# Optimization experiments

Measured on AMD Instinct MI355X. Metric: run time of the kernel, lower is better.

The kernel has to match this reference:

```python
import jax, jax.numpy as jnp
import numpy as np

N_NODES = 50000


def gcn_conv(x, W, b, edge_index, n):
    # PyG GCNConv(add_self_loops=False): h = x @ W; out[c] = sum_e norm_e * h[row_e]
    # with norm_e = deg(row)^-1/2 * deg(col)^-1/2, deg = in-degree on col.
    h = x @ W  # [N, out]
    row, col = edge_index[0], edge_index[1]
    deg = jax.ops.segment_sum(jnp.ones(row.shape, h.dtype), col, num_segments=n)
    dis = jnp.where(deg > 0, jax.lax.rsqrt(jnp.where(deg > 0, deg, 1.0)), 0.0)
    norm = dis[row] * dis[col]  # [E]
    msg = h[row] * norm[:, None]  # [E, out]
    out = jax.ops.segment_sum(msg, col, num_segments=n)
    return out + b


def setup_inputs() -> dict:
    key = jax.random.key(0)
    ks = jax.random.split(key, 12)
    N, F, H0, H1, H2, C = N_NODES, 512, 256, 128, 128, 40
    E1, E2 = 800000, 1600000
    s = 0.05
    return {
        "x": jax.random.normal(ks[0], (N, F), jnp.float32),
        "edge_index": jax.random.randint(ks[1], (2, E1), 0, N, jnp.int32),
        "edge_index2": jax.random.randint(ks[2], (2, E2), 0, N, jnp.int32),
        "W_lin1": jax.random.normal(ks[3], (F, H0), jnp.float32) * s,
        "b_lin1": jnp.zeros((H0,), jnp.float32),
        "W_c1": jax.random.normal(ks[4], (H0, H1), jnp.float32) * s,
        "b_c1": jnp.zeros((H1,), jnp.float32),
        "W_c2": jax.random.normal(ks[5], (2 * H1, H2), jnp.float32) * s,
        "b_c2": jnp.zeros((H2,), jnp.float32),
        "W_lin2": jax.random.normal(ks[6], (H0 + 2 * H1 + 2 * H2, C), jnp.float32) * s,
        "b_lin2": jnp.zeros((C,), jnp.float32),
    }


def reference(x, edge_index, edge_index2, W_lin1, b_lin1, W_c1, b_c1, W_c2, b_c2, W_lin2, b_lin2):
    n = x.shape[0]
    h = jax.nn.relu(x @ W_lin1 + b_lin1)  # [N, H0]
    first_hop_h = gcn_conv(h, W_c1, b_c1, edge_index, n)
    second_hop_h = gcn_conv(h, W_c1, b_c1, edge_index2, n)
    R1 = jnp.concatenate([first_hop_h, second_hop_h], axis=1)  # [N, 2*H1]
    first_hop_h2 = gcn_conv(R1, W_c2, b_c2, edge_index, n)
    second_hop_h2 = gcn_conv(R1, W_c2, b_c2, edge_index2, n)
    R2 = jnp.concatenate([first_hop_h2, second_hop_h2], axis=1)  # [N, 2*H2]
    final_h = jnp.concatenate([h, R1, R2], axis=1)  # [N, H0+2H1+2H2]
    # dropout treated as identity (eval / deterministic reference)
    logits = final_h @ W_lin2 + b_lin2
    return jax.nn.log_softmax(logits, axis=1)
```

## Files before the change

kernel.cpp:

```cpp
#include <hip/hip_runtime.h>
#include <hip/hip_bf16.h>
#include <stdint.h>

typedef __attribute__((ext_vector_type(8))) short bf16x8;
typedef __attribute__((ext_vector_type(8))) unsigned short ushort8v;
typedef __attribute__((ext_vector_type(4))) float f32x4;
typedef __attribute__((ext_vector_type(2))) float f32x2;
typedef __attribute__((ext_vector_type(4))) unsigned int u32x4;
typedef unsigned long long ull;

__device__ __forceinline__ void load_lds16(const void* g, void* l){
  __builtin_amdgcn_global_load_lds((const __attribute__((address_space(1))) void*)g,
                                   (__attribute__((address_space(3))) void*)l, 16, 0, 0);
}

__device__ __forceinline__ float bf2f(unsigned int u){
  union { unsigned int i; float f; } x; x.i = u << 16; return x.f;
}
__device__ __forceinline__ unsigned short f2bf(float f){
  __hip_bfloat16 h = __float2bfloat16(f);
  unsigned short u;
  __builtin_memcpy(&u, &h, 2);
  return u;
}

__global__ void wtrans4_kernel(const float* __restrict__ W1, unsigned short* __restrict__ Wt1,
                               const float* __restrict__ Wc1, unsigned short* __restrict__ Wtc1,
                               const float* __restrict__ Wc2, unsigned short* __restrict__ Wtc2,
                               const float* __restrict__ Wf, unsigned short* __restrict__ Wtf,
                               int NB, int cap1r, int cap2r, int* __restrict__ bcur,
                               unsigned* __restrict__ Tz0, unsigned* __restrict__ Tz1){
  int idx = blockIdx.x*256 + threadIdx.x;
  if (idx >= 245760){
    int i = idx - 245760;
    if (i < NB) bcur[i] = i*cap1r;
    else if (i < 2*NB) bcur[i] = NB*cap1r + (i - NB)*cap2r;
    else if (i < 2*NB + 32) Tz0[i - 2*NB] = 0u;
    else if (i < 2*NB + 64) Tz1[i - 2*NB - 32] = 0u;
    return;
  }
  const float* W; unsigned short* Wt; int K, N;
  if (idx < 131072){ W = W1; Wt = Wt1; K = 512; N = 256; }
  else if (idx < 163840){ idx -= 131072; W = Wc1; Wt = Wtc1; K = 256; N = 128; }
  else if (idx < 196608){ idx -= 163840; W = Wc2; Wt = Wtc2; K = 256; N = 128; }
  else { idx -= 196608; W = Wf; Wt = Wtf; K = 768; N = 40; }
  int nn = idx / K, kk = idx - nn*K;
  float v = (nn < N) ? W[(size_t)kk*N + nn] : 0.f;
  Wt[idx] = f2bf(v);
}

#define PCH 4096

__global__ __launch_bounds__(256) void partA_kernel(
    const int* __restrict__ ei1, int E1, const int* __restrict__ ei2, int E2,
    int* __restrict__ bcur, unsigned* __restrict__ staging, int NB)
{
  const int set = blockIdx.y;
  const int* __restrict__ ei = set ? ei2 : ei1;
  const int E = set ? E2 : E1;
  int* __restrict__ cur = bcur + set*NB;
  __shared__ int hist[400];
  __shared__ int resv[400];
  const int tid = threadIdx.x;
  const int base = blockIdx.x * PCH;
  if (base >= E) return;
  for (int b = tid; b < NB; b += 256) hist[b] = 0;
  __syncthreads();

  if (base + PCH <= E){
    const int t0 = base + tid*16;
    int4 c[4], r[4];
    #pragma unroll
    for (int j = 0; j < 4; ++j) c[j] = *(const int4*)(ei + E + t0 + j*4);
    #pragma unroll
    for (int j = 0; j < 4; ++j) r[j] = *(const int4*)(ei + t0 + j*4);
    #pragma unroll
    for (int j = 0; j < 4; ++j){
      atomicAdd(&hist[c[j].x >> 7], 1); atomicAdd(&hist[c[j].y >> 7], 1);
      atomicAdd(&hist[c[j].z >> 7], 1); atomicAdd(&hist[c[j].w >> 7], 1);
    }
    __syncthreads();
    for (int b = tid; b < NB; b += 256){
      int hc = hist[b];
      resv[b] = hc ? atomicAdd(&cur[b], hc) : 0;
      hist[b] = 0;
    }
    __syncthreads();
    #pragma unroll
    for (int j = 0; j < 4; ++j){
      int cc, rr, b, s;
      cc = c[j].x; rr = r[j].x; b = cc >> 7;
      s = resv[b] + atomicAdd(&hist[b], 1);
      staging[s] = ((unsigned)rr << 7) | (unsigned)(cc & 127);
      cc = c[j].y; rr = r[j].y; b = cc >> 7;
      s = resv[b] + atomicAdd(&hist[b], 1);
      staging[s] = ((unsigned)rr << 7) | (unsigned)(cc & 127);
      cc = c[j].z; rr = r[j].z; b = cc >> 7;
      s = resv[b] + atomicAdd(&hist[b], 1);
      staging[s] = ((unsigned)rr << 7) | (unsigned)(cc & 127);
      cc = c[j].w; rr = r[j].w; b = cc >> 7;
      s = resv[b] + atomicAdd(&hist[b], 1);
      staging[s] = ((unsigned)rr << 7) | (unsigned)(cc & 127);
    }
  } else {
    for (int i = 0; i < PCH/256; ++i){
      int e = base + i*256 + tid;
      if (e < E) atomicAdd(&hist[ei[E + e] >> 7], 1);
    }
    __syncthreads();
    for (int b = tid; b < NB; b += 256){
      int hc = hist[b];
      resv[b] = hc ? atomicAdd(&cur[b], hc) : 0;
      hist[b] = 0;
    }
    __syncthreads();
    for (int i = 0; i < PCH/256; ++i){
      int e = base + i*256 + tid;
      if (e < E){
        int c = ei[E + e], r = ei[e];
        int b = c >> 7;
        int s = resv[b] + atomicAdd(&hist[b], 1);
        staging[s] = ((unsigned)r << 7) | (unsigned)(c & 127);
      }
    }
  }
}

__global__ __launch_bounds__(256) void degB_kernel(
    const unsigned* __restrict__ staging, const int* __restrict__ bcur,
    int* __restrict__ deg1, int* __restrict__ deg2,
    float* __restrict__ dis1, float* __restrict__ dis2,
    int NB, int n, int cap1r, int cap2r)
{
  const int set = blockIdx.y;
  int* __restrict__ deg = set ? deg2 : deg1;
  float* __restrict__ dis = set ? dis2 : dis1;
  const int b = blockIdx.x;
  const int nodebase = b << 7;
  const int nn = min(128, n - nodebase);
  if (nn <= 0) return;
  __shared__ int cnt[128];
  const int tid = threadIdx.x;
  if (tid < 128) cnt[tid] = 0;
  __syncthreads();
  const int s0 = set ? (NB*cap1r + b*cap2r) : (b*cap1r);
  const int s1 = bcur[set*NB + b];
  for (int i = s0 + tid; i < s1; i += 256)
    atomicAdd(&cnt[staging[i] & 127], 1);
  __syncthreads();
  if (tid < nn){
    int c = cnt[tid];
    deg[nodebase + tid] = c;
    dis[nodebase + tid] = (c > 0) ? (1.0f/sqrtf((float)c)) : 0.f;
  }
}

__global__ void scan1_kernel(const int* __restrict__ deg1, const int* __restrict__ deg2,
                             int* __restrict__ off1, int* __restrict__ off2,
                             int* __restrict__ bsum, int n){
  __shared__ int s[1024];
  int set = blockIdx.y;
  const int* deg = set ? deg2 : deg1;
  int* off = set ? off2 : off1;
  int tid = threadIdx.x;
  int i = blockIdx.x*1024 + tid;
  int v = (i < n) ? ((deg[i] + 7) & ~7) : 0;
  s[tid] = v;
  __syncthreads();
  for (int o = 1; o < 1024; o <<= 1){
    int t = (tid >= o) ? s[tid - o] : 0;
    __syncthreads();
    s[tid] += t;
    __syncthreads();
  }
  if (i < n) off[i] = s[tid];
  if (tid == 1023) bsum[set*64 + blockIdx.x] = s[1023];
}

__global__ void scan2_kernel(const int* __restrict__ bsum, int* __restrict__ bbase,
                             int nch, int* __restrict__ off1, int* __restrict__ off2, int n){
  int set = threadIdx.x;
  if (set < 2){
    int run = 0;
    for (int j = 0; j < nch; ++j){ bbase[set*64 + j] = run; run += bsum[set*64 + j]; }
    (set ? off2 : off1)[n] = run;
  }
}

__global__ void scan3_kernel(const int* __restrict__ deg1, const int* __restrict__ deg2,
                             int* __restrict__ off1, int* __restrict__ off2,
                             const int* __restrict__ bbase, int n){
  int set = blockIdx.y;
  const int* deg = set ? deg2 : deg1;
  int* off = set ? off2 : off1;
  int i = blockIdx.x*1024 + threadIdx.x;
  if (i < n){
    int e = off[i] + bbase[set*64 + blockIdx.x];
    off[i] = e - ((deg[i] + 7) & ~7);
  }
}

__global__ __launch_bounds__(256) void partB_kernel(
    const unsigned* __restrict__ staging, const int* __restrict__ bcur,
    const int* __restrict__ off1, const int* __restrict__ off2,
    unsigned* __restrict__ csr1, unsigned* __restrict__ csr2,
    int NB, int n, unsigned padrow, int cap1r, int cap2r)
{
  const int set = blockIdx.y;
  const int* __restrict__ off = set ? off2 : off1;
  unsigned* __restrict__ csr = set ? csr2 : csr1;
  const int b = blockIdx.x;
  const int nodebase = b << 7;
  const int nn = min(128, n - nodebase);
  if (nn <= 0) return;
  __shared__ int offv[129];
  __shared__ int curl[128];
  const int tid = threadIdx.x;
  if (tid <= nn) offv[tid] = off[nodebase + tid];
  if (tid < 128) curl[tid] = 0;
  __syncthreads();
  const int s0 = set ? (NB*cap1r + b*cap2r) : (b*cap1r);
  const int s1 = bcur[set*NB + b];
  for (int i = s0 + tid; i < s1; i += 256){
    unsigned v = staging[i];
    int cl = v & 127;
    int p = offv[cl] + atomicAdd(&curl[cl], 1);
    csr[p] = v >> 7;
  }
  __syncthreads();
  for (int c = tid; c < nn; c += 256){
    int p1 = offv[c+1];
    for (int p = offv[c] + curl[c]; p < p1; ++p) csr[p] = padrow;
  }
  if (b == 0 && tid < 64) csr[off[n] + tid] = padrow;
}

#define KN 8
__global__ __launch_bounds__(256) void conv_kernel(
    const int* __restrict__ off1, const unsigned* __restrict__ csr1, const float* __restrict__ dis1,
    const int* __restrict__ off2, const unsigned* __restrict__ csr2, const float* __restrict__ dis2,
    const unsigned char* __restrict__ Tbase,
    const float* __restrict__ bias, unsigned short* __restrict__ outR,
    int n, int ntab)
{
  const int set = blockIdx.y;
  const int* __restrict__ off = set ? off2 : off1;
  const float* __restrict__ dis = set ? dis2 : dis1;
  const unsigned* __restrict__ csrq = set ? csr2 : csr1;
  const int col_ofs = set ? 128 : 0;
  const unsigned* __restrict__ tab =
      (const unsigned*)(Tbase + (size_t)set * ntab * 128);

  const int wv0 = (blockIdx.x*4 + (threadIdx.x >> 6)) * KN;
  if (wv0 >= n) return;
  const int wend = min(n, wv0 + KN);
  const int l = threadIdx.x & 63;
  const int half = l >> 5, lf = l & 31;
  const float b0 = bias[lf*4 + 0], b1 = bias[lf*4 + 1];
  const float b2 = bias[lf*4 + 2], b3 = bias[lf*4 + 3];

  const int offs = off[wv0 + min(l, wend - wv0)];
  const int cstart = __shfl(offs, 0, 64);
  const int pend   = __shfl(offs, wend - wv0, 64);
  int node = wv0;
  int nxt  = __shfl(offs, min(1, wend - wv0), 64);

  float ax = 0.f, ay = 0.f, az = 0.f, aw = 0.f;

#define EMIT_NODE { \
    float rx = ax + __shfl_xor(ax, 32, 64); \
    float ry = ay + __shfl_xor(ay, 32, 64); \
    float rz = az + __shfl_xor(az, 32, 64); \
    float rw = aw + __shfl_xor(aw, 32, 64); \
    if (half == 0){ \
      const float dc = dis[node]; \
      ull ov = (ull)((unsigned)f2bf(fmaf(dc, rx, b0)) | ((unsigned)f2bf(fmaf(dc, ry, b1)) << 16)) \
             | ((ull)((unsigned)f2bf(fmaf(dc, rz, b2)) | ((unsigned)f2bf(fmaf(dc, rw, b3)) << 16)) << 32); \
      __builtin_nontemporal_store(ov, (ull*)&outR[(size_t)node*256 + col_ofs + lf*4]); \
    } \
    ax = ay = az = aw = 0.f; }
#define DRAIN(CUR) \
    while (node < wend && (CUR) == nxt){ \
      EMIT_NODE \
      ++node; \
      nxt = __shfl(offs, min(node + 1 - wv0, KN), 64); \
    }

  DRAIN(cstart)

  const int nbat = (pend - cstart) >> 3;
  if (nbat > 0){
    const unsigned* cp = csrq + cstart + half*4;
    u32x4 qa, qb;
    unsigned va0, va1, va2, va3, vb0, vb1, vb2, vb3;

#define LQ(q, B) q = __builtin_nontemporal_load((const u32x4*)(cp + (B)*8));
#define GATH(v, q) \
    v##0 = tab[(size_t)q.x * 32 + lf]; \
    v##1 = tab[(size_t)q.y * 32 + lf]; \
    v##2 = tab[(size_t)q.z * 32 + lf]; \
    v##3 = tab[(size_t)q.w * 32 + lf];
#define FMA1(v) { \
    f32x2 lo = __builtin_amdgcn_cvt_pk_f32_fp8((int)v, false); \
    f32x2 hi = __builtin_amdgcn_cvt_pk_f32_fp8((int)v, true);  \
    ax += lo.x; ay += lo.y; az += hi.x; aw += hi.y; }
#define FMAB(v) { FMA1(v##0) FMA1(v##1) FMA1(v##2) FMA1(v##3) }

    LQ(qa, 0)
    GATH(va, qa)
    LQ(qb, 1)
    int b = 0;
    while (b + 2 <= nbat){
      LQ(qa, b + 2)
      GATH(vb, qb)
      FMAB(va)
      DRAIN(cstart + (b + 1)*8)
      LQ(qb, b + 3)
      GATH(va, qa)
      FMAB(vb)
      DRAIN(cstart + (b + 2)*8)
      b += 2;
    }
    if (b < nbat){
      FMAB(va)
      DRAIN(cstart + nbat*8)
    }
#undef LQ
#undef GATH
#undef FMA1
#undef FMAB
  }
  while (node < wend){ EMIT_NODE ++node; }
#undef EMIT_NODE
#undef DRAIN
}

template<int FM, int FN, int WGM, int WGN, int EPI, bool AF32>
__global__ __launch_bounds__(WGM*WGN*64, (WGM*WGN*64) == 512 ? 4 : 2) void gemm_kernel(
    const unsigned short* __restrict__ A0, const float* __restrict__ Af,
    const unsigned short* __restrict__ A1, const unsigned short* __restrict__ A2,
    const unsigned short* __restrict__ Bt, const float* __restrict__ bias,
    void* __restrict__ Cout, int M, int K, int lda, int ldc,
    const float* __restrict__ d1, const float* __restrict__ d2, int ntab)
{
  constexpr int THREADS = WGM*WGN*64;
  constexpr int BM = WGM*FM*16;
  constexpr int BN = WGN*FN*16;
  constexpr int BK = 32;
  constexpr int AJ = (BM*BK/8)/THREADS;
  constexpr int BJ = (BN*BK/8)/THREADS;
  static_assert(BM == 128, "staging assumes BM==128");
  __shared__ unsigned short As[BM][BK];
  __shared__ unsigned short Bs[BN][BK];
  const int tid = threadIdx.x;
  const int w = tid >> 6, l = tid & 63;
  const int wr = w / WGN, wc = w % WGN;
  const int m0 = blockIdx.x*BM, n0 = blockIdx.y*BN;
  f32x4 acc[FM][FN] = {};
  const int nsteps = K / BK;
  for (int s = 0; s < nsteps; ++s){
    const int k0 = s*BK;
    const unsigned short* Asrc = A0;
    int kin = k0;
    if constexpr (EPI == 2){
      int slab = k0 >> 8;
      Asrc = (slab == 0) ? A0 : ((slab == 1) ? A1 : A2);
      kin = k0 & 255;
    }
    __syncthreads();
    if constexpr (AF32){
      #pragma unroll
      for (int j = 0; j < AJ; ++j){
        int idx = j*THREADS + tid;
        int row = idx >> 2, kq = idx & 3;
        int rg = m0 + row; rg = (rg < M) ? rg : (M - 1);
        const float* src = Af + (size_t)rg*lda + kin + kq*8;
        float4 a = *(const float4*)src;
        float4 b2 = *(const float4*)(src + 4);
        ushort8v u;
        u[0] = f2bf(a.x);  u[1] = f2bf(a.y);  u[2] = f2bf(a.z);  u[3] = f2bf(a.w);
        u[4] = f2bf(b2.x); u[5] = f2bf(b2.y); u[6] = f2bf(b2.z); u[7] = f2bf(b2.w);
        *(ushort8v*)((char*)&As[0][0] + (size_t)idx*16) = u;
      }
    } else {
      #pragma unroll
      for (int j = 0; j < AJ; ++j){
        int idx = j*THREADS + tid;
        int row = idx >> 2, kq = idx & 3;
        int rg = m0 + row; rg = (rg < M) ? rg : (M - 1);
        load_lds16(Asrc + (size_t)rg*lda + kin + kq*8,
                   ((char*)&As[0][0]) + (size_t)(j*THREADS + w*64)*16);
      }
    }
    #pragma unroll
    for (int j = 0; j < BJ; ++j){
      int idx = j*THREADS + tid;
      int row = idx >> 2, kq = idx & 3;
      load_lds16(Bt + (size_t)(n0 + row)*K + k0 + kq*8,
                 ((char*)&Bs[0][0]) + (size_t)(j*THREADS + w*64)*16);
    }
    __syncthreads();
    bf16x8 af[FM], bfr[FN];
    const int kofs = (l >> 4)*8, l16 = l & 15;
    #pragma unroll
    for (int mi = 0; mi < FM; ++mi)
      af[mi] = *(const bf16x8*)&As[wr*FM*16 + mi*16 + l16][kofs];
    #pragma unroll
    for (int ni = 0; ni < FN; ++ni)
      bfr[ni] = *(const bf16x8*)&Bs[wc*FN*16 + ni*16 + l16][kofs];
    #pragma unroll
    for (int mi = 0; mi < FM; ++mi)
      #pragma unroll
      for (int ni = 0; ni < FN; ++ni)
        acc[mi][ni] = __builtin_amdgcn_mfma_f32_16x16x32_bf16(af[mi], bfr[ni], acc[mi][ni], 0, 0, 0);
  }
  const int lg = l >> 4, lc = l & 15;
  if constexpr (EPI == 2){
    float* O = (float*)Cout;
    #pragma unroll
    for (int mi = 0; mi < FM; ++mi){
      #pragma unroll
      for (int i = 0; i < 4; ++i){
        int row = m0 + wr*FM*16 + mi*16 + lg*4 + i;
        float v[FN];
        float mx = -1e30f;
        #pragma unroll
        for (int ni = 0; ni < FN; ++ni){
          int col = ni*16 + lc;
          v[ni] = acc[mi][ni][i] + ((col < 40) ? bias[col] : 0.f);
          if (col < 40) mx = fmaxf(mx, v[ni]);
        }
        #pragma unroll
        for (int d = 1; d < 16; d <<= 1) mx = fmaxf(mx, __shfl_xor(mx, d, 64));
        float se = 0.f;
        #pragma unroll
        for (int ni = 0; ni < FN; ++ni){
          int col = ni*16 + lc;
          if (col < 40) se += expf(v[ni] - mx);
        }
        #pragma unroll
        for (int d = 1; d < 16; d <<= 1) se += __shfl_xor(se, d, 64);
        float lse = logf(se);
        if (row < M){
          #pragma unroll
          for (int ni = 0; ni < FN; ++ni){
            int col = ni*16 + lc;
            if (col < 40) O[(size_t)row*40 + col] = v[ni] - mx - lse;
          }
        }
      }
    }
  } else if constexpr (EPI == 4){
    unsigned char* T = (unsigned char*)Cout;
    #pragma unroll
    for (int mi = 0; mi < FM; ++mi){
      #pragma unroll
      for (int i = 0; i < 4; ++i){
        int row = m0 + wr*FM*16 + mi*16 + lg*4 + i;
        if (row >= M) continue;
        float s1 = d1[row], s2 = d2[row];
        #pragma unroll
        for (int ni = 0; ni < FN; ++ni){
          int col = n0 + wc*FN*16 + ni*16 + lc;
          float vv = acc[mi][ni][i];
          unsigned p1 = (unsigned)__builtin_amdgcn_cvt_pk_fp8_f32(vv*s1, vv*s1, 0, false);
          unsigned p2 = (unsigned)__builtin_amdgcn_cvt_pk_fp8_f32(vv*s2, vv*s2, 0, false);
          T[(size_t)row*128 + col] = (unsigned char)(p1 & 0xff);
          T[((size_t)ntab + row)*128 + col] = (unsigned char)(p2 & 0xff);
        }
      }
    }
  } else {
    unsigned short* C = (unsigned short*)Cout;
    #pragma unroll
    for (int mi = 0; mi < FM; ++mi){
      #pragma unroll
      for (int i = 0; i < 4; ++i){
        int row = m0 + wr*FM*16 + mi*16 + lg*4 + i;
        if (row >= M) continue;
        #pragma unroll
        for (int ni = 0; ni < FN; ++ni){
          int col = n0 + wc*FN*16 + ni*16 + lc;
          float vv = acc[mi][ni][i];
          if constexpr (EPI == 1){ vv += bias[col]; vv = fmaxf(vv, 0.f); }
          C[(size_t)row*ldc + col] = f2bf(vv);
        }
      }
    }
  }
}

extern "C" void kernel_launch(void* const* d_in, const int* in_sizes, int n_in,
                              void* d_out, int out_size, void* d_ws, size_t ws_size,
                              hipStream_t stream)
{
  (void)n_in; (void)out_size;
  const float* x      = (const float*)d_in[0];
  const int*   ei1    = (const int*)d_in[1];
  const int*   ei2    = (const int*)d_in[2];
  const float* W_lin1 = (const float*)d_in[3];
  const float* b_lin1 = (const float*)d_in[4];
  const float* W_c1   = (const float*)d_in[5];
  const float* b_c1   = (const float*)d_in[6];
  const float* W_c2   = (const float*)d_in[7];
  const float* b_c2   = (const float*)d_in[8];
  const float* W_lin2 = (const float*)d_in[9];
  const float* b_lin2 = (const float*)d_in[10];

  const int N  = in_sizes[0] / 512;
  const int E1 = in_sizes[1] / 2;
  const int E2 = in_sizes[2] / 2;
  const int ntab = N + 1;
  const int NB = (N + 127) >> 7;
  const int cap1r = (((E1 + NB - 1)/NB + 768) + 63) & ~63;
  const int cap2r = (((E2 + NB - 1)/NB + 1536) + 63) & ~63;

  char* base = (char*)d_ws;
  size_t off = 0;
  auto alloc = [&](size_t bytes) -> char* {
    off = (off + 255) & ~(size_t)255;
    char* r = base + off;
    off += bytes;
    return r;
  };
  const size_t cap1 = (size_t)E1 + 8*(size_t)N + 64;
  const size_t cap2 = (size_t)E2 + 8*(size_t)N + 64;

  unsigned short* h    = (unsigned short*)alloc((size_t)N*256*2);
  unsigned char*  T    = (unsigned char*)alloc((size_t)2*ntab*128);
  unsigned short* R1   = (unsigned short*)alloc((size_t)N*256*2);
  unsigned short* R2   = (unsigned short*)alloc((size_t)N*256*2);
  unsigned short* Wt1  = (unsigned short*)alloc((size_t)256*512*2);
  unsigned short* Wtc1 = (unsigned short*)alloc((size_t)128*256*2);
  unsigned short* Wtc2 = (unsigned short*)alloc((size_t)128*256*2);
  unsigned short* Wtf  = (unsigned short*)alloc((size_t)64*768*2);
  int* degblk = (int*)alloc((size_t)2*N*4);
  int* deg1 = degblk, *deg2 = degblk + N;
  float* dis1 = (float*)alloc((size_t)N*4);
  float* dis2 = (float*)alloc((size_t)N*4);
  int* off1 = (int*)alloc((size_t)(N+1)*4);
  int* off2 = (int*)alloc((size_t)(N+1)*4);
  int* bsum  = (int*)alloc(128*4);
  int* bbase = (int*)alloc(128*4);
  int* bcur  = (int*)alloc((size_t)2*NB*4);
  unsigned* csr1 = (unsigned*)alloc(cap1*4);
  unsigned* csr2 = (unsigned*)alloc(cap2*4);
  unsigned* staging = (unsigned*)alloc((size_t)NB*((size_t)cap1r + cap2r)*4);
  if (off > ws_size) return;

  int mt = (N + 127)/128;
  int nwv = (N + KN - 1)/KN;
  int cb = (nwv + 3)/4;

  wtrans4_kernel<<<(245760 + 2*NB + 64 + 255)/256, 256, 0, stream>>>(
      W_lin1, Wt1, W_c1, Wtc1, W_c2, Wtc2, W_lin2, Wtf,
      NB, cap1r, cap2r, bcur,
      (unsigned*)(T + (size_t)N*128), (unsigned*)(T + ((size_t)ntab + N)*128));
  gemm_kernel<4,4,2,4,1,true><<<dim3(mt, 1), 512, 0, stream>>>(
      nullptr, x, nullptr, nullptr, Wt1, b_lin1, h, N, 512, 512, 256, nullptr, nullptr, 0);

  partA_kernel<<<dim3((E2 + PCH - 1)/PCH, 2), 256, 0, stream>>>(ei1, E1, ei2, E2, bcur, staging, NB);
  degB_kernel<<<dim3(NB, 2), 256, 0, stream>>>(staging, bcur, deg1, deg2, dis1, dis2,
                                               NB, N, cap1r, cap2r);
  int nch = (N + 1023)/1024;
  scan1_kernel<<<dim3(nch, 2), 1024, 0, stream>>>(deg1, deg2, off1, off2, bsum, N);
  scan2_kernel<<<1, 64, 0, stream>>>(bsum, bbase, nch, off1, off2, N);
  scan3_kernel<<<dim3(nch, 2), 1024, 0, stream>>>(deg1, deg2, off1, off2, bbase, N);
  partB_kernel<<<dim3(NB, 2), 256, 0, stream>>>(staging, bcur, off1, off2, csr1, csr2,
                                                NB, N, (unsigned)N, cap1r, cap2r);

  gemm_kernel<4,4,2,2,4,false><<<dim3(mt, 1), 256, 0, stream>>>(
      h, nullptr, nullptr, nullptr, Wtc1, nullptr, T, N, 256, 256, 0, dis1, dis2, ntab);
  conv_kernel<<<dim3(cb, 2), 256, 0, stream>>>(off1, csr1, dis1, off2, csr2, dis2,
                                               T, b_c1, R1, N, ntab);
  gemm_kernel<4,4,2,2,4,false><<<dim3(mt, 1), 256, 0, stream>>>(
      R1, nullptr, nullptr, nullptr, Wtc2, nullptr, T, N, 256, 256, 0, dis1, dis2, ntab);
  conv_kernel<<<dim3(cb, 2), 256, 0, stream>>>(off1, csr1, dis1, off2, csr2, dis2,
                                               T, b_c2, R2, N, ntab);
  gemm_kernel<2,4,4,1,2,false><<<dim3(mt, 1), 256, 0, stream>>>(
      h, nullptr, R1, R2, Wtf, b_lin2, d_out, N, 768, 256, 40, nullptr, nullptr, 0);
}
```

Before: 248.2 us.

## Fuse degree count, scan and CSR partition into one per-bucket kernel

The degree, three-pass global scan and partition kernels are merged into a single kernel. Each 128-node bucket counts its degrees, does a local prefix scan in LDS, and writes its CSR into a fixed-capacity per-bucket segment with per-bucket offsets (129 entries). This removes four launches and the global deg/off round trips. The conv kernel now indexes the blocked offset array instead. The per-bucket capacity is a statistical bound (mean plus a multiple of its square root), which could overflow on skewed degree distributions.

```diff
diff --git a/kernel.cpp b/kernel.cpp
--- a/kernel.cpp
+++ b/kernel.cpp
@@ -1,6 +1,7 @@
 #include <hip/hip_runtime.h>
 #include <hip/hip_bf16.h>
 #include <stdint.h>
+#include <math.h>
 
 typedef __attribute__((ext_vector_type(8))) short bf16x8;
 typedef __attribute__((ext_vector_type(8))) unsigned short ushort8v;
@@ -126,20 +127,25 @@
   }
 }
 
-__global__ __launch_bounds__(256) void degB_kernel(
+__global__ __launch_bounds__(256) void degpartB_kernel(
     const unsigned* __restrict__ staging, const int* __restrict__ bcur,
-    int* __restrict__ deg1, int* __restrict__ deg2,
     float* __restrict__ dis1, float* __restrict__ dis2,
-    int NB, int n, int cap1r, int cap2r)
+    int* __restrict__ goff1, int* __restrict__ goff2,
+    unsigned* __restrict__ csr1, unsigned* __restrict__ csr2,
+    int NB, int n, unsigned padrow, int cap1r, int cap2r, int capb1, int capb2)
 {
   const int set = blockIdx.y;
-  int* __restrict__ deg = set ? deg2 : deg1;
   float* __restrict__ dis = set ? dis2 : dis1;
+  int* __restrict__ goff = set ? goff2 : goff1;
+  unsigned* __restrict__ csr = set ? csr2 : csr1;
+  const int capb = set ? capb2 : capb1;
   const int b = blockIdx.x;
   const int nodebase = b << 7;
   const int nn = min(128, n - nodebase);
   if (nn <= 0) return;
   __shared__ int cnt[128];
+  __shared__ int offv[129];
+  __shared__ int curl[128];
   const int tid = threadIdx.x;
   if (tid < 128) cnt[tid] = 0;
   __syncthreads();
@@ -148,79 +154,29 @@
   for (int i = s0 + tid; i < s1; i += 256)
     atomicAdd(&cnt[staging[i] & 127], 1);
   __syncthreads();
+  int pc = 0;
+  if (tid < 128){ pc = (cnt[tid] + 7) & ~7; curl[tid] = pc; }
+  __syncthreads();
+  for (int o = 1; o < 128; o <<= 1){
+    int t = 0;
+    if (tid < 128 && tid >= o) t = curl[tid - o];
+    __syncthreads();
+    if (tid < 128) curl[tid] += t;
+    __syncthreads();
+  }
+  const int cbase = b * capb;
+  if (tid < 128){
+    offv[tid] = cbase + curl[tid] - pc;
+    if (tid == 127) offv[128] = cbase + curl[127];
+  }
+  __syncthreads();
+  if (tid <= 128) goff[b*129 + tid] = offv[tid];
   if (tid < nn){
     int c = cnt[tid];
-    deg[nodebase + tid] = c;
     dis[nodebase + tid] = (c > 0) ? (1.0f/sqrtf((float)c)) : 0.f;
   }
-}
-
-__global__ void scan1_kernel(const int* __restrict__ deg1, const int* __restrict__ deg2,
-                             int* __restrict__ off1, int* __restrict__ off2,
-                             int* __restrict__ bsum, int n){
-  __shared__ int s[1024];
-  int set = blockIdx.y;
-  const int* deg = set ? deg2 : deg1;
-  int* off = set ? off2 : off1;
-  int tid = threadIdx.x;
-  int i = blockIdx.x*1024 + tid;
-  int v = (i < n) ? ((deg[i] + 7) & ~7) : 0;
-  s[tid] = v;
-  __syncthreads();
-  for (int o = 1; o < 1024; o <<= 1){
-    int t = (tid >= o) ? s[tid - o] : 0;
-    __syncthreads();
-    s[tid] += t;
-    __syncthreads();
-  }
-  if (i < n) off[i] = s[tid];
-  if (tid == 1023) bsum[set*64 + blockIdx.x] = s[1023];
-}
-
-__global__ void scan2_kernel(const int* __restrict__ bsum, int* __restrict__ bbase,
-                             int nch, int* __restrict__ off1, int* __restrict__ off2, int n){
-  int set = threadIdx.x;
-  if (set < 2){
-    int run = 0;
-    for (int j = 0; j < nch; ++j){ bbase[set*64 + j] = run; run += bsum[set*64 + j]; }
-    (set ? off2 : off1)[n] = run;
-  }
-}
-
-__global__ void scan3_kernel(const int* __restrict__ deg1, const int* __restrict__ deg2,
-                             int* __restrict__ off1, int* __restrict__ off2,
-                             const int* __restrict__ bbase, int n){
-  int set = blockIdx.y;
-  const int* deg = set ? deg2 : deg1;
-  int* off = set ? off2 : off1;
-  int i = blockIdx.x*1024 + threadIdx.x;
-  if (i < n){
-    int e = off[i] + bbase[set*64 + blockIdx.x];
-    off[i] = e - ((deg[i] + 7) & ~7);
-  }
-}
-
-__global__ __launch_bounds__(256) void partB_kernel(
-    const unsigned* __restrict__ staging, const int* __restrict__ bcur,
-    const int* __restrict__ off1, const int* __restrict__ off2,
-    unsigned* __restrict__ csr1, unsigned* __restrict__ csr2,
-    int NB, int n, unsigned padrow, int cap1r, int cap2r)
-{
-  const int set = blockIdx.y;
-  const int* __restrict__ off = set ? off2 : off1;
-  unsigned* __restrict__ csr = set ? csr2 : csr1;
-  const int b = blockIdx.x;
-  const int nodebase = b << 7;
-  const int nn = min(128, n - nodebase);
-  if (nn <= 0) return;
-  __shared__ int offv[129];
-  __shared__ int curl[128];
-  const int tid = threadIdx.x;
-  if (tid <= nn) offv[tid] = off[nodebase + tid];
   if (tid < 128) curl[tid] = 0;
   __syncthreads();
-  const int s0 = set ? (NB*cap1r + b*cap2r) : (b*cap1r);
-  const int s1 = bcur[set*NB + b];
   for (int i = s0 + tid; i < s1; i += 256){
     unsigned v = staging[i];
     int cl = v & 127;
@@ -228,23 +184,23 @@
     csr[p] = v >> 7;
   }
   __syncthreads();
-  for (int c = tid; c < nn; c += 256){
-    int p1 = offv[c+1];
-    for (int p = offv[c] + curl[c]; p < p1; ++p) csr[p] = padrow;
-  }
-  if (b == 0 && tid < 64) csr[off[n] + tid] = padrow;
+  for (int c = tid; c < 128; c += 256){
+    int p1 = offv[c + 1];
+    for (int p = offv[c] + cnt[c]; p < p1; ++p) csr[p] = padrow;
+  }
+  if (tid < 64) csr[offv[128] + tid] = padrow;
 }
 
 #define KN 8
 __global__ __launch_bounds__(256) void conv_kernel(
-    const int* __restrict__ off1, const unsigned* __restrict__ csr1, const float* __restrict__ dis1,
-    const int* __restrict__ off2, const unsigned* __restrict__ csr2, const float* __restrict__ dis2,
+    const int* __restrict__ goff1, const unsigned* __restrict__ csr1, const float* __restrict__ dis1,
+    const int* __restrict__ goff2, const unsigned* __restrict__ csr2, const float* __restrict__ dis2,
     const unsigned char* __restrict__ Tbase,
     const float* __restrict__ bias, unsigned short* __restrict__ outR,
     int n, int ntab)
 {
   const int set = blockIdx.y;
-  const int* __restrict__ off = set ? off2 : off1;
+  const int* __restrict__ goff = set ? goff2 : goff1;
   const float* __restrict__ dis = set ? dis2 : dis1;
   const unsigned* __restrict__ csrq = set ? csr2 : csr1;
   const int col_ofs = set ? 128 : 0;
@@ -259,7 +215,8 @@
   const float b0 = bias[lf*4 + 0], b1 = bias[lf*4 + 1];
   const float b2 = bias[lf*4 + 2], b3 = bias[lf*4 + 3];
 
-  const int offs = off[wv0 + min(l, wend - wv0)];
+  const int gbase = (wv0 >> 7)*129 + (wv0 & 127);
+  const int offs = goff[gbase + min(l, wend - wv0)];
   const int cstart = __shfl(offs, 0, 64);
   const int pend   = __shfl(offs, wend - wv0, 64);
   int node = wv0;
@@ -514,6 +471,9 @@
   const int NB = (N + 127) >> 7;
   const int cap1r = (((E1 + NB - 1)/NB + 768) + 63) & ~63;
   const int cap2r = (((E2 + NB - 1)/NB + 1536) + 63) & ~63;
+  const int mb1 = (int)(128.0*E1/N), mb2 = (int)(128.0*E2/N);
+  const int capb1 = (mb1 + (int)(17.0*sqrt((double)mb1)) + 896 + 64 + 63) & ~63;
+  const int capb2 = (mb2 + (int)(17.0*sqrt((double)mb2)) + 896 + 64 + 63) & ~63;
 
   char* base = (char*)d_ws;
   size_t off = 0;
@@ -523,8 +483,6 @@
     off += bytes;
     return r;
   };
-  const size_t cap1 = (size_t)E1 + 8*(size_t)N + 64;
-  const size_t cap2 = (size_t)E2 + 8*(size_t)N + 64;
 
   unsigned short* h    = (unsigned short*)alloc((size_t)N*256*2);
   unsigned char*  T    = (unsigned char*)alloc((size_t)2*ntab*128);
@@ -534,17 +492,13 @@
   unsigned short* Wtc1 = (unsigned short*)alloc((size_t)128*256*2);
   unsigned short* Wtc2 = (unsigned short*)alloc((size_t)128*256*2);
   unsigned short* Wtf  = (unsigned short*)alloc((size_t)64*768*2);
-  int* degblk = (int*)alloc((size_t)2*N*4);
-  int* deg1 = degblk, *deg2 = degblk + N;
   float* dis1 = (float*)alloc((size_t)N*4);
   float* dis2 = (float*)alloc((size_t)N*4);
-  int* off1 = (int*)alloc((size_t)(N+1)*4);
-  int* off2 = (int*)alloc((size_t)(N+1)*4);
-  int* bsum  = (int*)alloc(128*4);
-  int* bbase = (int*)alloc(128*4);
+  int* goff1 = (int*)alloc((size_t)NB*129*4);
+  int* goff2 = (int*)alloc((size_t)NB*129*4);
   int* bcur  = (int*)alloc((size_t)2*NB*4);
-  unsigned* csr1 = (unsigned*)alloc(cap1*4);
-  unsigned* csr2 = (unsigned*)alloc(cap2*4);
+  unsigned* csr1 = (unsigned*)alloc((size_t)NB*capb1*4);
+  unsigned* csr2 = (unsigned*)alloc((size_t)NB*capb2*4);
   unsigned* staging = (unsigned*)alloc((size_t)NB*((size_t)cap1r + cap2r)*4);
   if (off > ws_size) return;
 
@@ -560,22 +514,17 @@
       nullptr, x, nullptr, nullptr, Wt1, b_lin1, h, N, 512, 512, 256, nullptr, nullptr, 0);
 
   partA_kernel<<<dim3((E2 + PCH - 1)/PCH, 2), 256, 0, stream>>>(ei1, E1, ei2, E2, bcur, staging, NB);
-  degB_kernel<<<dim3(NB, 2), 256, 0, stream>>>(staging, bcur, deg1, deg2, dis1, dis2,
-                                               NB, N, cap1r, cap2r);
-  int nch = (N + 1023)/1024;
-  scan1_kernel<<<dim3(nch, 2), 1024, 0, stream>>>(deg1, deg2, off1, off2, bsum, N);
-  scan2_kernel<<<1, 64, 0, stream>>>(bsum, bbase, nch, off1, off2, N);
-  scan3_kernel<<<dim3(nch, 2), 1024, 0, stream>>>(deg1, deg2, off1, off2, bbase, N);
-  partB_kernel<<<dim3(NB, 2), 256, 0, stream>>>(staging, bcur, off1, off2, csr1, csr2,
-                                                NB, N, (unsigned)N, cap1r, cap2r);
+  degpartB_kernel<<<dim3(NB, 2), 256, 0, stream>>>(staging, bcur, dis1, dis2, goff1, goff2,
+                                                   csr1, csr2, NB, N, (unsigned)N,
+                                                   cap1r, cap2r, capb1, capb2);
 
   gemm_kernel<4,4,2,2,4,false><<<dim3(mt, 1), 256, 0, stream>>>(
       h, nullptr, nullptr, nullptr, Wtc1, nullptr, T, N, 256, 256, 0, dis1, dis2, ntab);
-  conv_kernel<<<dim3(cb, 2), 256, 0, stream>>>(off1, csr1, dis1, off2, csr2, dis2,
+  conv_kernel<<<dim3(cb, 2), 256, 0, stream>>>(goff1, csr1, dis1, goff2, csr2, dis2,
                                                T, b_c1, R1, N, ntab);
   gemm_kernel<4,4,2,2,4,false><<<dim3(mt, 1), 256, 0, stream>>>(
       R1, nullptr, nullptr, nullptr, Wtc2, nullptr, T, N, 256, 256, 0, dis1, dis2, ntab);
-  conv_kernel<<<dim3(cb, 2), 256, 0, stream>>>(off1, csr1, dis1, off2, csr2, dis2,
+  conv_kernel<<<dim3(cb, 2), 256, 0, stream>>>(goff1, csr1, dis1, goff2, csr2, dis2,
                                                T, b_c2, R2, N, ntab);
   gemm_kernel<2,4,4,1,2,false><<<dim3(mt, 1), 256, 0, stream>>>(
       h, nullptr, R1, R2, Wtf, b_lin2, d_out, N, 768, 256, 40, nullptr, nullptr, 0);
```

After: 236.8 us, median of 2. 1.05x faster.
